# Kernel tuning notes

Measured on AMD Instinct MI355X. Metric: run time of the kernel, lower is better.

## Reference

```python
import jax, jax.numpy as jnp
import numpy as np

T, H, E, I, K = 1024, 1024, 16, 512, 4   # tokens, hidden, n_experts, expert ffn dim, top_k
IS = 1024                                 # shared-experts intermediate = n_shared(2) * I
LIMIT = 7.0                               # swiglu_limit
SCALE = 2.5                               # routed_scaling_factor
VOCAB = 32000


def setup_inputs() -> dict:
    key = jax.random.key(0)
    ks = jax.random.split(key, 10)
    sh = 1.0 / np.sqrt(H)
    si = 1.0 / np.sqrt(I)
    ss = 1.0 / np.sqrt(IS)
    x = jax.random.normal(ks[0], (T, H), jnp.float32)
    input_ids = jax.random.randint(ks[1], (T,), 0, VOCAB)
    Wg = jax.random.normal(ks[2], (E, H), jnp.float32) * sh          # gate (router), fp32
    bias = jax.random.normal(ks[3], (E,), jnp.float32) * 0.1         # e_score_correction_bias
    W1 = jax.random.normal(ks[4], (E, H, I), jnp.float32) * sh       # expert gate proj
    W3 = jax.random.normal(ks[5], (E, H, I), jnp.float32) * sh       # expert up proj
    W2 = jax.random.normal(ks[6], (E, I, H), jnp.float32) * si       # expert down proj
    Wsg = jax.random.normal(ks[7], (H, IS), jnp.float32) * sh        # shared gate proj
    Wsu = jax.random.normal(ks[8], (H, IS), jnp.float32) * sh        # shared up proj
    Wsd = jax.random.normal(ks[9], (IS, H), jnp.float32) * ss        # shared down proj
    return {"hidden_states": x, "input_ids": input_ids, "Wg": Wg, "bias": bias,
            "W1": W1, "W3": W3, "W2": W2, "Wsg": Wsg, "Wsu": Wsu, "Wsd": Wsd}


def reference(hidden_states, input_ids, Wg, bias, W1, W3, W2, Wsg, Wsu, Wsd):
    x = hidden_states  # [T, H]
    # --- router (fp32 logits, sqrtsoftplus scoring, noaux_tc top-k with correction bias) ---
    logits = jnp.einsum('th,eh->te', x.astype(jnp.float32), Wg)       # [T, E]
    scores = jnp.sqrt(jax.nn.softplus(logits))                         # sqrtsoftplus
    _, topi = jax.lax.top_k(scores + bias[None, :], K)                 # select with bias
    w = jnp.take_along_axis(scores, topi, axis=1)                      # weights from raw scores
    w = w / jnp.sum(w, axis=1, keepdims=True) * SCALE                  # renormalize + scale
    # dense [T, E] combine weights (zero for unselected experts)
    w_dense = jnp.zeros((T, E), x.dtype).at[jnp.arange(T)[:, None], topi].add(w.astype(x.dtype))
    # --- routed experts: clamped swiglu (gpt-oss style, per swiglu_limit) ---
    g = jnp.einsum('th,ehi->tei', x, W1)                               # [T, E, I]
    u = jnp.einsum('th,ehi->tei', x, W3)
    g = jnp.clip(g, None, LIMIT)
    u = jnp.clip(u, -LIMIT, LIMIT)
    act = (g * jax.nn.sigmoid(1.702 * g)) * (u + 1.0)
    routed = jnp.einsum('tei,eih,te->th', act, W2, w_dense)            # weighted combine
    # --- shared experts: standard SiLU-gated MLP ---
    shared = (jax.nn.silu(x @ Wsg) * (x @ Wsu)) @ Wsd
    return routed + shared
```

## Files before the change

### kernel.cpp

```cpp
#include <hip/hip_runtime.h>
#include <hip/hip_bf16.h>
#include <math.h>

#define T_ 1024
#define H_ 1024
#define E_ 16
#define I_ 512
#define KSEL 4
#define IS_ 1024

typedef unsigned short u16;
typedef __attribute__((ext_vector_type(8))) short short8;
typedef __attribute__((ext_vector_type(4))) float f32x4;

__device__ __forceinline__ u16 f2bf(float f) {
    union { float f; unsigned int u; } v; v.f = f;
    unsigned int u = v.u;
    return (u16)((u + 0x7fffu + ((u >> 16) & 1u)) >> 16);
}
__device__ __forceinline__ float bf2f(u16 b) {
    union { unsigned int u; float f; } v; v.u = ((unsigned int)b) << 16;
    return v.f;
}
__device__ __forceinline__ unsigned cvtpk(float lo, float hi) {
    unsigned r;
    asm("v_cvt_pk_bf16_f32 %0, %1, %2" : "=v"(r) : "v"(lo), "v"(hi));
    return r;
}
__device__ __forceinline__ void gload16(const u16* g, u16* l) {
    __builtin_amdgcn_global_load_lds(
        (const __attribute__((address_space(1))) void*)g,
        (__attribute__((address_space(3))) void*)l, 16, 0, 0);
}
__device__ __forceinline__ void SB0() { __builtin_amdgcn_sched_barrier(0); }
__device__ __forceinline__ void BARRIER() {
    asm volatile("s_waitcnt lgkmcnt(0)" ::: "memory");
    __builtin_amdgcn_s_barrier();
    __builtin_amdgcn_sched_barrier(0);
}

__global__ __launch_bounds__(256)
void router_kernel(const float* __restrict__ x, const float* __restrict__ Wg,
                   const float* __restrict__ bias, int* __restrict__ counts,
                   int* __restrict__ tok_list, int* __restrict__ slot_list,
                   float* __restrict__ wt_dense, u16* __restrict__ x_bf, int cap) {
    __shared__ float part[4][16];
    int t = blockIdx.x;
    int tid = threadIdx.x;
    int e = tid & 15;
    int q = tid >> 4;
    const float4* xv = (const float4*)(x + (long)t * H_) + q * 16;
    const float4* wv = (const float4*)(Wg + (long)e * H_) + q * 16;
    float d = 0.f;
#pragma unroll
    for (int i = 0; i < 16; i++) {
        float4 a = xv[i], b = wv[i];
        d += a.x * b.x + a.y * b.y + a.z * b.z + a.w * b.w;
    }
    d += __shfl_down(d, 16);
    d += __shfl_down(d, 32);
    if ((tid & 63) < 16) part[tid >> 6][e] = d;
    {
        float4 v = ((const float4*)(x + (long)t * H_))[tid];
        ushort4 o;
        o.x = f2bf(v.x); o.y = f2bf(v.y); o.z = f2bf(v.z); o.w = f2bf(v.w);
        ((ushort4*)(x_bf + (long)t * H_))[tid] = o;
    }
    __syncthreads();
    if (tid >= 64) return;
    int lane = tid;
    float lg = part[0][e] + part[1][e] + part[2][e] + part[3][e];
    float sp = fmaxf(lg, 0.f) + log1pf(expf(-fabsf(lg)));
    float s = sqrtf(sp);
    float bs = s + bias[e];
    int sel[KSEL]; float ssel[KSEL]; float wsum = 0.f;
#pragma unroll
    for (int k = 0; k < KSEL; k++) {
        float mv = bs; int me = e;
#pragma unroll
        for (int off = 1; off < 16; off <<= 1) {
            float ov = __shfl_xor(mv, off);
            int oe = __shfl_xor(me, off);
            if (ov > mv || (ov == mv && oe < me)) { mv = ov; me = oe; }
        }
        sel[k] = me;
        float sk = __shfl(s, (lane & 48) | me);
        ssel[k] = sk; wsum += sk;
        if (e == me) bs = -1e30f;
    }
    float inv = 2.5f / wsum;
    if (lane < KSEL) {
        int k = lane;
        int se = sel[k];
        wt_dense[t * KSEL + k] = ssel[k] * inv;
        int pos = atomicAdd(&counts[se], 1);
        if (pos < cap) {
            tok_list[se * T_ + pos] = t;
            slot_list[se * T_ + pos] = t * KSEL + k;
        }
    }
}

struct Seg {
    const u16* A; const int* gather;
    const float* B0; const float* B1;
    void* C; const int* scatter; const int* counts;
    long sAe, sBe, sCe;
    int lda, ldb, ldc;
    int il, cf32, act, nt, nxt, mt, nE, cap, Mfull;
};

__global__ __launch_bounds__(256, 2)
void moe_gemm(Seg sa, Seg sb) {
    int id = blockIdx.x;
    int n0 = sa.nxt * sa.mt * sa.nE;
    Seg s = (id < n0) ? sa : sb;
    int rid = (id < n0) ? id : id - n0;
    int per = s.nxt * s.mt;
    int e = rid / per;
    int r2 = rid - e * per;
    int my = r2 / s.nxt;
    int nx = r2 - my * s.nxt;
    int Mlim = s.counts ? (s.counts[e] < s.cap ? s.counts[e] : s.cap) : s.Mfull;
    int mbase = my * 128;
    if (mbase >= Mlim) return;
    int nbase = nx * 128;
    int nt = s.nt;

    __shared__ __align__(16) u16 lds[40960];
    u16* a0 = lds;
    u16* a1 = lds + 8192;
    u16* a2 = lds + 16384;
    u16* Bb0 = lds + 24576;
    u16* Bb1 = lds + 32768;

    int tid = threadIdx.x, lane = tid & 63, wid = tid >> 6;

    const u16* Abase = s.A + (long)e * s.sAe;
    const int* gat = s.gather ? s.gather + e * T_ : nullptr;
    const u16* aptr[4];
    {
        int srow = tid >> 3;
        int kc = (tid & 7) ^ (srow & 7);
#pragma unroll
        for (int j = 0; j < 4; j++) {
            int gr = mbase + srow + j * 32;
            int grc = gr < Mlim ? gr : (Mlim - 1);
            long ar = gat ? (long)gat[grc] : (long)grc;
            aptr[j] = Abase + ar * (long)s.lda + kc * 8;
        }
    }
    int adoff = tid * 8;

    int cg = tid & 31, kc = tid >> 5;
    const float* bp;
    {
        int pc = nbase + cg * 4;
        if (s.il) {
            int chunk = pc >> 4;
            const float* src = (chunk & 1) ? s.B1 : s.B0;
            bp = src + (long)e * s.sBe + ((chunk >> 1) * 16 + (pc & 15));
        } else {
            bp = s.B0 + (long)e * s.sBe + pc;
        }
        bp += (long)(kc * 8) * s.ldb;
    }
    long ldbl = s.ldb;
    f32x4 bA[8], bB[8];

    auto issueA = [&](u16* ab, int kt) {
#pragma unroll
        for (int j = 0; j < 4; j++)
            gload16(aptr[j] + kt * 64, ab + adoff + j * 2048);
    };
    auto issueB = [&](f32x4 (&b)[8], int kt) {
        const float* r = bp + (long)(kt * 64) * ldbl;
#pragma unroll
        for (int i = 0; i < 8; i++)
            b[i] = *(const f32x4*)(r + (long)i * ldbl);
    };
    auto cvtw = [&](f32x4 (&b)[8], u16* bb) {
#pragma unroll
        for (int j = 0; j < 4; j++) {
            int row = cg * 4 + j;
            uint4 v;
            v.x = cvtpk(b[0][j], b[1][j]);
            v.y = cvtpk(b[2][j], b[3][j]);
            v.z = cvtpk(b[4][j], b[5][j]);
            v.w = cvtpk(b[6][j], b[7][j]);
            *(uint4*)(bb + row * 64 + ((kc ^ (row & 7)) << 3)) = v;
        }
    };

    int wm = wid >> 1, wn = wid & 1, lr = lane & 15, lk = lane >> 4;
    f32x4 acc[4][4] = {};
    auto compute = [&](const u16* ab, const u16* bb) {
#pragma unroll
        for (int kk = 0; kk < 2; kk++) {
            short8 afr[4], bfr[4];
#pragma unroll
            for (int mi = 0; mi < 4; mi++) {
                int R = wm * 64 + mi * 16 + lr;
                afr[mi] = *(const short8*)(ab + R * 64 + (((kk * 4 + lk) ^ (R & 7)) << 3));
            }
#pragma unroll
            for (int ni = 0; ni < 4; ni++) {
                int R = wn * 64 + ni * 16 + lr;
                bfr[ni] = *(const short8*)(bb + R * 64 + (((kk * 4 + lk) ^ (R & 7)) << 3));
            }
#pragma unroll
            for (int mi = 0; mi < 4; mi++)
#pragma unroll
                for (int ni = 0; ni < 4; ni++)
                    acc[mi][ni] = __builtin_amdgcn_mfma_f32_16x16x32_bf16(afr[mi], bfr[ni], acc[mi][ni], 0, 0, 0);
        }
    };

    issueA(a0, 0); SB0(); issueB(bA, 0); SB0();
    issueA(a1, 1); SB0(); issueB(bB, 1); SB0();
    cvtw(bA, Bb0);
    BARRIER();

    for (int t = 0; t < nt; t += 2) {
        if (t + 2 < nt) { issueA(a2, t + 2); SB0(); issueB(bA, t + 2); SB0(); }
        compute(a0, Bb0);
        cvtw(bB, Bb1);
        BARRIER();
        if (t + 3 < nt) { issueA(a0, t + 3); SB0(); issueB(bB, t + 3); SB0(); }
        compute(a1, Bb1);
        if (t + 2 < nt) { cvtw(bA, Bb0); BARRIER(); }
        u16* tmp = a0; a0 = a2; a2 = a1; a1 = tmp;
    }

    if (s.act == 0) {
        u16* Cb = (u16*)s.C;
        float* Cf = (float*)s.C;
        long cbase = s.scatter ? 0L : (long)e * s.sCe;
        const int* scat = s.scatter ? s.scatter + e * T_ : nullptr;
#pragma unroll
        for (int mi = 0; mi < 4; mi++) {
#pragma unroll
            for (int j = 0; j < 4; j++) {
                int rowt = wm * 64 + mi * 16 + lk * 4 + j;
                int gr = mbase + rowt;
                if (gr >= Mlim) continue;
                long crow = scat ? (long)scat[gr] : (long)gr;
                long rb = cbase + crow * (long)s.ldc;
#pragma unroll
                for (int ni = 0; ni < 4; ni++) {
                    int col = nbase + wn * 64 + ni * 16 + lr;
                    float v = acc[mi][ni][j];
                    if (s.cf32) Cf[rb + col] = v;
                    else        Cb[rb + col] = f2bf(v);
                }
            }
        }
    } else {
        u16* Co = (u16*)s.C;
        long cbase = (long)e * s.sCe;
#pragma unroll
        for (int mi = 0; mi < 4; mi++) {
#pragma unroll
            for (int j = 0; j < 4; j++) {
                int rowt = wm * 64 + mi * 16 + lk * 4 + j;
                int gr = mbase + rowt;
                if (gr >= Mlim) continue;
                long rb = cbase + (long)gr * s.ldc;
#pragma unroll
                for (int q = 0; q < 2; q++) {
                    int ocol = (nbase >> 1) + wn * 32 + q * 16 + lr;
                    float g = acc[mi][2 * q][j];
                    float u = acc[mi][2 * q + 1][j];
                    float r;
                    if (s.act == 1) {
                        r = g / (1.f + expf(-g)) * u;
                    } else {
                        g = fminf(g, 7.f);
                        u = fminf(fmaxf(u, -7.f), 7.f);
                        r = g / (1.f + expf(-1.702f * g)) * (u + 1.f);
                    }
                    Co[rb + ocol] = f2bf(r);
                }
            }
        }
    }
}

__global__ void final_add_kernel(float* __restrict__ out, const u16* __restrict__ down,
                                 const float* __restrict__ wtd) {
    int i = blockIdx.x * blockDim.x + threadIdx.x;
    int o = i * 4;
    int t = o >> 10;
    int h = o & (H_ - 1);
    float4 w4 = *(const float4*)(wtd + t * 4);
    float wk[4] = {w4.x, w4.y, w4.z, w4.w};
    float4 v = ((float4*)out)[i];
#pragma unroll
    for (int k = 0; k < KSEL; k++) {
        const u16* dr = down + ((long)(t * KSEL + k) << 10) + h;
        ushort4 d4 = *(const ushort4*)dr;
        v.x += wk[k] * bf2f(d4.x);
        v.y += wk[k] * bf2f(d4.y);
        v.z += wk[k] * bf2f(d4.z);
        v.w += wk[k] * bf2f(d4.w);
    }
    ((float4*)out)[i] = v;
}

extern "C" void kernel_launch(void* const* d_in, const int* in_sizes, int n_in,
                              void* d_out, int out_size, void* d_ws, size_t ws_size,
                              hipStream_t stream) {
    const float* x    = (const float*)d_in[0];
    const float* Wg   = (const float*)d_in[2];
    const float* bias = (const float*)d_in[3];
    const float* W1   = (const float*)d_in[4];
    const float* W3   = (const float*)d_in[5];
    const float* W2   = (const float*)d_in[6];
    const float* Wsg  = (const float*)d_in[7];
    const float* Wsu  = (const float*)d_in[8];
    const float* Wsd  = (const float*)d_in[9];
    float* out = (float*)d_out;
    char* ws = (char*)d_ws;

    size_t off = 0;
    auto carve = [&](size_t bytes) -> char* {
        char* p = ws + off;
        off = (off + bytes + 255) & ~(size_t)255;
        return p;
    };
    u16* x_bf   = (u16*)carve((size_t)T_ * H_ * 2);
    u16* c1     = (u16*)carve((size_t)T_ * IS_ * 2);
    u16* dwn    = (u16*)carve((size_t)T_ * KSEL * H_ * 2);
    int* counts    = (int*)carve(E_ * sizeof(int));
    int* tok_list  = (int*)carve((size_t)E_ * T_ * 4);
    int* slot_list = (int*)carve((size_t)E_ * T_ * 4);
    float* wt_dense = (float*)carve((size_t)T_ * KSEL * 4);

    long cap = 768;
    int capB = (int)(cap / 128);
    u16* act = (u16*)carve((size_t)E_ * cap * I_ * 2);

    hipMemsetAsync(counts, 0, E_ * sizeof(int), stream);
    router_kernel<<<T_, 256, 0, stream>>>(x, Wg, bias, counts, tok_list, slot_list,
                                          wt_dense, x_bf, (int)cap);

    Seg eu;
    eu.A = x_bf; eu.gather = tok_list; eu.B0 = W1; eu.B1 = W3;
    eu.C = (void*)act; eu.scatter = nullptr; eu.counts = counts;
    eu.sAe = 0; eu.sBe = (long)H_ * I_; eu.sCe = (long)cap * I_;
    eu.lda = H_; eu.ldb = I_; eu.ldc = I_;
    eu.il = 1; eu.cf32 = 0; eu.act = 2; eu.nt = 16;
    eu.nxt = 8; eu.mt = capB; eu.nE = E_; eu.cap = (int)cap; eu.Mfull = 0;
    Seg su;
    su.A = x_bf; su.gather = nullptr; su.B0 = Wsg; su.B1 = Wsu;
    su.C = (void*)c1; su.scatter = nullptr; su.counts = nullptr;
    su.sAe = 0; su.sBe = 0; su.sCe = 0;
    su.lda = H_; su.ldb = IS_; su.ldc = IS_;
    su.il = 1; su.cf32 = 0; su.act = 1; su.nt = 16;
    su.nxt = 16; su.mt = 8; su.nE = 1; su.cap = 0; su.Mfull = T_;
    int upBlocks = eu.nxt * eu.mt * eu.nE + su.nxt * su.mt * su.nE;
    moe_gemm<<<upBlocks, 256, 0, stream>>>(eu, su);

    Seg ed;
    ed.A = act; ed.gather = nullptr; ed.B0 = W2; ed.B1 = W2;
    ed.C = (void*)dwn; ed.scatter = slot_list; ed.counts = counts;
    ed.sAe = (long)cap * I_; ed.sBe = (long)I_ * H_; ed.sCe = 0;
    ed.lda = I_; ed.ldb = H_; ed.ldc = H_;
    ed.il = 0; ed.cf32 = 0; ed.act = 0; ed.nt = 8;
    ed.nxt = 8; ed.mt = capB; ed.nE = E_; ed.cap = (int)cap; ed.Mfull = 0;
    Seg sd;
    sd.A = c1; sd.gather = nullptr; sd.B0 = Wsd; sd.B1 = Wsd;
    sd.C = (void*)out; sd.scatter = nullptr; sd.counts = nullptr;
    sd.sAe = 0; sd.sBe = 0; sd.sCe = 0;
    sd.lda = IS_; sd.ldb = H_; sd.ldc = H_;
    sd.il = 0; sd.cf32 = 1; sd.act = 0; sd.nt = 16;
    sd.nxt = 8; sd.mt = 8; sd.nE = 1; sd.cap = 0; sd.Mfull = T_;
    int dnBlocks = ed.nxt * ed.mt * ed.nE + sd.nxt * sd.mt * sd.nE;
    moe_gemm<<<dnBlocks, 256, 0, stream>>>(ed, sd);

    final_add_kernel<<<T_ * H_ / 4 / 256, 256, 0, stream>>>(out, dwn, wt_dense);
}
```

Before: 93.65 us.

## Pre-transpose weights to bf16 and simplify GEMM to double-buffered LDS loads

Adds a transpose_conv kernel that converts all fp32 expert and shared weights into transposed bf16 buffers each call. The GEMM then loads both A and B via direct global-to-LDS loads with a simpler K=32 double-buffered loop, replacing the earlier register-staged fp32 B conversion, swizzled LDS layout and triple buffering. This removes the in-GEMM conversion work but adds a full extra read and write pass over the weights every call. The new unswizzled LDS layout may also cause bank conflicts.

Measured after the change: 127.8 us. 36.4% more time.

```diff
diff --git a/kernel.cpp b/kernel.cpp
--- a/kernel.cpp
+++ b/kernel.cpp
@@ -22,21 +22,10 @@
     union { unsigned int u; float f; } v; v.u = ((unsigned int)b) << 16;
     return v.f;
 }
-__device__ __forceinline__ unsigned cvtpk(float lo, float hi) {
-    unsigned r;
-    asm("v_cvt_pk_bf16_f32 %0, %1, %2" : "=v"(r) : "v"(lo), "v"(hi));
-    return r;
-}
 __device__ __forceinline__ void gload16(const u16* g, u16* l) {
     __builtin_amdgcn_global_load_lds(
         (const __attribute__((address_space(1))) void*)g,
         (__attribute__((address_space(3))) void*)l, 16, 0, 0);
-}
-__device__ __forceinline__ void SB0() { __builtin_amdgcn_sched_barrier(0); }
-__device__ __forceinline__ void BARRIER() {
-    asm volatile("s_waitcnt lgkmcnt(0)" ::: "memory");
-    __builtin_amdgcn_s_barrier();
-    __builtin_amdgcn_sched_barrier(0);
 }
 
 __global__ __launch_bounds__(256)
@@ -101,16 +90,54 @@
     }
 }
 
+__global__ __launch_bounds__(256)
+void transpose_conv(const float* __restrict__ s0, const float* __restrict__ s1,
+                    u16* __restrict__ out, int ldin, int ldout,
+                    long sIn, long sOut, int nE, int il) {
+    int z = blockIdx.z;
+    const float* src; int e, ofs;
+    if (il && z >= nE) { src = s1; e = z - nE; ofs = 16; }
+    else               { src = s0; e = z;      ofs = 0;  }
+    const float* ip = src + (long)e * sIn;
+    u16* op = out + (long)e * sOut;
+    __shared__ u16 tile[64 * 72];
+    int rb = blockIdx.y * 64, cb = blockIdx.x * 64;
+    int tid = threadIdx.x;
+    int r0 = (tid >> 4) * 4;
+    int c4 = (tid & 15) * 4;
+#pragma unroll
+    for (int i = 0; i < 4; i++) {
+        float4 v = *(const float4*)(ip + (long)(rb + r0 + i) * ldin + cb + c4);
+        ushort4 o;
+        o.x = f2bf(v.x); o.y = f2bf(v.y); o.z = f2bf(v.z); o.w = f2bf(v.w);
+        *(ushort4*)&tile[(r0 + i) * 72 + c4] = o;
+    }
+    __syncthreads();
+    int c = tid >> 2;
+    int r16 = (tid & 3) * 16;
+    short8 a, b;
+#pragma unroll
+    for (int j = 0; j < 8; j++) {
+        a[j] = (short)tile[(r16 + j) * 72 + c];
+        b[j] = (short)tile[(r16 + 8 + j) * 72 + c];
+    }
+    int cg = cb + c;
+    int orow = il ? (((cg >> 4) << 5) + (cg & 15) + ofs) : cg;
+    u16* orp = op + (long)orow * ldout + rb + r16;
+    *(short8*)(orp) = a;
+    *(short8*)(orp + 8) = b;
+}
+
 struct Seg {
     const u16* A; const int* gather;
-    const float* B0; const float* B1;
+    const u16* Bt;
     void* C; const int* scatter; const int* counts;
     long sAe, sBe, sCe;
     int lda, ldb, ldc;
-    int il, cf32, act, nt, nxt, mt, nE, cap, Mfull;
+    int cf32, act, nt, nxt, mt, nE, cap, Mfull;
 };
 
-__global__ __launch_bounds__(256, 2)
+__global__ __launch_bounds__(256)
 void moe_gemm(Seg sa, Seg sb) {
     int id = blockIdx.x;
     int n0 = sa.nxt * sa.mt * sa.nE;
@@ -125,111 +152,61 @@
     int mbase = my * 128;
     if (mbase >= Mlim) return;
     int nbase = nx * 128;
-    int nt = s.nt;
-
-    __shared__ __align__(16) u16 lds[40960];
-    u16* a0 = lds;
-    u16* a1 = lds + 8192;
-    u16* a2 = lds + 16384;
-    u16* Bb0 = lds + 24576;
-    u16* Bb1 = lds + 32768;
+
+    __shared__ __align__(16) u16 As[2][128 * 32];
+    __shared__ __align__(16) u16 Bs[2][128 * 32];
 
     int tid = threadIdx.x, lane = tid & 63, wid = tid >> 6;
-
     const u16* Abase = s.A + (long)e * s.sAe;
+    const u16* Bbase = s.Bt + (long)e * s.sBe;
     const int* gat = s.gather ? s.gather + e * T_ : nullptr;
-    const u16* aptr[4];
-    {
-        int srow = tid >> 3;
-        int kc = (tid & 7) ^ (srow & 7);
-#pragma unroll
-        for (int j = 0; j < 4; j++) {
-            int gr = mbase + srow + j * 32;
-            int grc = gr < Mlim ? gr : (Mlim - 1);
-            long ar = gat ? (long)gat[grc] : (long)grc;
-            aptr[j] = Abase + ar * (long)s.lda + kc * 8;
-        }
-    }
-    int adoff = tid * 8;
-
-    int cg = tid & 31, kc = tid >> 5;
-    const float* bp;
-    {
-        int pc = nbase + cg * 4;
-        if (s.il) {
-            int chunk = pc >> 4;
-            const float* src = (chunk & 1) ? s.B1 : s.B0;
-            bp = src + (long)e * s.sBe + ((chunk >> 1) * 16 + (pc & 15));
-        } else {
-            bp = s.B0 + (long)e * s.sBe + pc;
-        }
-        bp += (long)(kc * 8) * s.ldb;
-    }
-    long ldbl = s.ldb;
-    f32x4 bA[8], bB[8];
-
-    auto issueA = [&](u16* ab, int kt) {
-#pragma unroll
-        for (int j = 0; j < 4; j++)
-            gload16(aptr[j] + kt * 64, ab + adoff + j * 2048);
-    };
-    auto issueB = [&](f32x4 (&b)[8], int kt) {
-        const float* r = bp + (long)(kt * 64) * ldbl;
-#pragma unroll
-        for (int i = 0; i < 8; i++)
-            b[i] = *(const f32x4*)(r + (long)i * ldbl);
-    };
-    auto cvtw = [&](f32x4 (&b)[8], u16* bb) {
-#pragma unroll
-        for (int j = 0; j < 4; j++) {
-            int row = cg * 4 + j;
-            uint4 v;
-            v.x = cvtpk(b[0][j], b[1][j]);
-            v.y = cvtpk(b[2][j], b[3][j]);
-            v.z = cvtpk(b[4][j], b[5][j]);
-            v.w = cvtpk(b[6][j], b[7][j]);
-            *(uint4*)(bb + row * 64 + ((kc ^ (row & 7)) << 3)) = v;
-        }
-    };
+    const u16 *aptr[2], *bptr[2];
+#pragma unroll
+    for (int r = 0; r < 2; r++) {
+        int chunk = tid + r * 256;
+        int row = chunk >> 2, slot = chunk & 3;
+        int gr = mbase + row;
+        int grc = gr < Mlim ? gr : (Mlim - 1);
+        long ar = gat ? (long)gat[grc] : (long)grc;
+        aptr[r] = Abase + ar * (long)s.lda + slot * 8;
+        bptr[r] = Bbase + (long)(nbase + row) * s.ldb + slot * 8;
+    }
 
     int wm = wid >> 1, wn = wid & 1, lr = lane & 15, lk = lane >> 4;
     f32x4 acc[4][4] = {};
-    auto compute = [&](const u16* ab, const u16* bb) {
-#pragma unroll
-        for (int kk = 0; kk < 2; kk++) {
-            short8 afr[4], bfr[4];
-#pragma unroll
-            for (int mi = 0; mi < 4; mi++) {
-                int R = wm * 64 + mi * 16 + lr;
-                afr[mi] = *(const short8*)(ab + R * 64 + (((kk * 4 + lk) ^ (R & 7)) << 3));
-            }
-#pragma unroll
-            for (int ni = 0; ni < 4; ni++) {
-                int R = wn * 64 + ni * 16 + lr;
-                bfr[ni] = *(const short8*)(bb + R * 64 + (((kk * 4 + lk) ^ (R & 7)) << 3));
-            }
-#pragma unroll
-            for (int mi = 0; mi < 4; mi++)
-#pragma unroll
-                for (int ni = 0; ni < 4; ni++)
-                    acc[mi][ni] = __builtin_amdgcn_mfma_f32_16x16x32_bf16(afr[mi], bfr[ni], acc[mi][ni], 0, 0, 0);
-        }
+    int nt = s.nt;
+
+    auto issue = [&](int t, int buf) {
+        int k0 = t * 32;
+        u16* ad = &As[buf][0] + tid * 8;
+        u16* bd = &Bs[buf][0] + tid * 8;
+        gload16(aptr[0] + k0, ad);
+        gload16(aptr[1] + k0, ad + 2048);
+        gload16(bptr[0] + k0, bd);
+        gload16(bptr[1] + k0, bd + 2048);
     };
 
-    issueA(a0, 0); SB0(); issueB(bA, 0); SB0();
-    issueA(a1, 1); SB0(); issueB(bB, 1); SB0();
-    cvtw(bA, Bb0);
-    BARRIER();
-
-    for (int t = 0; t < nt; t += 2) {
-        if (t + 2 < nt) { issueA(a2, t + 2); SB0(); issueB(bA, t + 2); SB0(); }
-        compute(a0, Bb0);
-        cvtw(bB, Bb1);
-        BARRIER();
-        if (t + 3 < nt) { issueA(a0, t + 3); SB0(); issueB(bB, t + 3); SB0(); }
-        compute(a1, Bb1);
-        if (t + 2 < nt) { cvtw(bA, Bb0); BARRIER(); }
-        u16* tmp = a0; a0 = a2; a2 = a1; a1 = tmp;
+    issue(0, 0);
+    __syncthreads();
+
+    for (int t = 0; t < nt; t++) {
+        int cur = t & 1;
+        if (t + 1 < nt) issue(t + 1, cur ^ 1);
+        const u16* Asc = &As[cur][0];
+        const u16* Bsc = &Bs[cur][0];
+        short8 afr[4], bfr[4];
+#pragma unroll
+        for (int mi = 0; mi < 4; mi++)
+            afr[mi] = *(const short8*)&Asc[(wm * 64 + mi * 16 + lr) * 32 + lk * 8];
+#pragma unroll
+        for (int ni = 0; ni < 4; ni++)
+            bfr[ni] = *(const short8*)&Bsc[(wn * 64 + ni * 16 + lr) * 32 + lk * 8];
+#pragma unroll
+        for (int mi = 0; mi < 4; mi++)
+#pragma unroll
+            for (int ni = 0; ni < 4; ni++)
+                acc[mi][ni] = __builtin_amdgcn_mfma_f32_16x16x32_bf16(afr[mi], bfr[ni], acc[mi][ni], 0, 0, 0);
+        __syncthreads();
     }
 
     if (s.act == 0) {
@@ -335,6 +312,10 @@
     int* tok_list  = (int*)carve((size_t)E_ * T_ * 4);
     int* slot_list = (int*)carve((size_t)E_ * T_ * 4);
     float* wt_dense = (float*)carve((size_t)T_ * KSEL * 4);
+    u16* W13t  = (u16*)carve((size_t)E_ * 1024 * 1024 * 2);
+    u16* Wsgut = (u16*)carve((size_t)2048 * 1024 * 2);
+    u16* W2t   = (u16*)carve((size_t)E_ * 1024 * 512 * 2);
+    u16* Wsdt  = (u16*)carve((size_t)1024 * 1024 * 2);
 
     long cap = 768;
     int capB = (int)(cap / 128);
@@ -344,39 +325,49 @@
     router_kernel<<<T_, 256, 0, stream>>>(x, Wg, bias, counts, tok_list, slot_list,
                                           wt_dense, x_bf, (int)cap);
 
+    dim3 blk(256);
+    transpose_conv<<<dim3(I_ / 64, H_ / 64, 2 * E_), blk, 0, stream>>>(
+        W1, W3, W13t, I_, H_, (long)H_ * I_, (long)1024 * 1024, E_, 1);
+    transpose_conv<<<dim3(IS_ / 64, H_ / 64, 2), blk, 0, stream>>>(
+        Wsg, Wsu, Wsgut, IS_, H_, 0, 0, 1, 1);
+    transpose_conv<<<dim3(H_ / 64, I_ / 64, E_), blk, 0, stream>>>(
+        W2, W2, W2t, H_, I_, (long)I_ * H_, (long)H_ * I_, E_, 0);
+    transpose_conv<<<dim3(H_ / 64, IS_ / 64, 1), blk, 0, stream>>>(
+        Wsd, Wsd, Wsdt, H_, IS_, 0, 0, 1, 0);
+
     Seg eu;
-    eu.A = x_bf; eu.gather = tok_list; eu.B0 = W1; eu.B1 = W3;
+    eu.A = x_bf; eu.gather = tok_list; eu.Bt = W13t;
     eu.C = (void*)act; eu.scatter = nullptr; eu.counts = counts;
-    eu.sAe = 0; eu.sBe = (long)H_ * I_; eu.sCe = (long)cap * I_;
-    eu.lda = H_; eu.ldb = I_; eu.ldc = I_;
-    eu.il = 1; eu.cf32 = 0; eu.act = 2; eu.nt = 16;
+    eu.sAe = 0; eu.sBe = (long)1024 * 1024; eu.sCe = (long)cap * I_;
+    eu.lda = H_; eu.ldb = H_; eu.ldc = I_;
+    eu.cf32 = 0; eu.act = 2; eu.nt = H_ / 32;
     eu.nxt = 8; eu.mt = capB; eu.nE = E_; eu.cap = (int)cap; eu.Mfull = 0;
     Seg su;
-    su.A = x_bf; su.gather = nullptr; su.B0 = Wsg; su.B1 = Wsu;
+    su.A = x_bf; su.gather = nullptr; su.Bt = Wsgut;
     su.C = (void*)c1; su.scatter = nullptr; su.counts = nullptr;
     su.sAe = 0; su.sBe = 0; su.sCe = 0;
-    su.lda = H_; su.ldb = IS_; su.ldc = IS_;
-    su.il = 1; su.cf32 = 0; su.act = 1; su.nt = 16;
+    su.lda = H_; su.ldb = H_; su.ldc = IS_;
+    su.cf32 = 0; su.act = 1; su.nt = H_ / 32;
     su.nxt = 16; su.mt = 8; su.nE = 1; su.cap = 0; su.Mfull = T_;
     int upBlocks = eu.nxt * eu.mt * eu.nE + su.nxt * su.mt * su.nE;
-    moe_gemm<<<upBlocks, 256, 0, stream>>>(eu, su);
+    moe_gemm<<<upBlocks, blk, 0, stream>>>(eu, su);
 
     Seg ed;
-    ed.A = act; ed.gather = nullptr; ed.B0 = W2; ed.B1 = W2;
+    ed.A = act; ed.gather = nullptr; ed.Bt = W2t;
     ed.C = (void*)dwn; ed.scatter = slot_list; ed.counts = counts;
-    ed.sAe = (long)cap * I_; ed.sBe = (long)I_ * H_; ed.sCe = 0;
-    ed.lda = I_; ed.ldb = H_; ed.ldc = H_;
-    ed.il = 0; ed.cf32 = 0; ed.act = 0; ed.nt = 8;
+    ed.sAe = (long)cap * I_; ed.sBe = (long)H_ * I_; ed.sCe = 0;
+    ed.lda = I_; ed.ldb = I_; ed.ldc = H_;
+    ed.cf32 = 0; ed.act = 0; ed.nt = I_ / 32;
     ed.nxt = 8; ed.mt = capB; ed.nE = E_; ed.cap = (int)cap; ed.Mfull = 0;
     Seg sd;
-    sd.A = c1; sd.gather = nullptr; sd.B0 = Wsd; sd.B1 = Wsd;
+    sd.A = c1; sd.gather = nullptr; sd.Bt = Wsdt;
     sd.C = (void*)out; sd.scatter = nullptr; sd.counts = nullptr;
     sd.sAe = 0; sd.sBe = 0; sd.sCe = 0;
-    sd.lda = IS_; sd.ldb = H_; sd.ldc = H_;
-    sd.il = 0; sd.cf32 = 1; sd.act = 0; sd.nt = 16;
+    sd.lda = IS_; sd.ldb = IS_; sd.ldc = H_;
+    sd.cf32 = 1; sd.act = 0; sd.nt = IS_ / 32;
     sd.nxt = 8; sd.mt = 8; sd.nE = 1; sd.cap = 0; sd.Mfull = T_;
     int dnBlocks = ed.nxt * ed.mt * ed.nE + sd.nxt * sd.mt * sd.nE;
-    moe_gemm<<<dnBlocks, 256, 0, stream>>>(ed, sd);
+    moe_gemm<<<dnBlocks, blk, 0, stream>>>(ed, sd);
 
     final_add_kernel<<<T_ * H_ / 4 / 256, 256, 0, stream>>>(out, dwn, wt_dense);
 }
```
